# Kernel tuning notes

Hardware: AMD Instinct MI355X
Metric: run time of the kernel (lower is better)

Reference implementation:

```python
import jax, jax.numpy as jnp
import numpy as np

H = 512      # hidden_size
OUT = 1      # output_size (forced by prev_output shape (B,1,1))
B = 64       # batch
T = 1024     # output_length


def setup_inputs() -> dict:
    key = jax.random.key(0)
    ks = jax.random.split(key, 10)
    s_in = 1.0 / np.sqrt(H)
    return {
        "context_vector": jax.random.normal(ks[0], (B, 1, H), jnp.float32),
        "expected_output": jax.random.normal(ks[1], (B, T, OUT), jnp.float32),
        "W_ih0": jax.random.normal(ks[2], (3 * H, H + OUT), jnp.float32) * s_in,
        "W_hh0": jax.random.normal(ks[3], (3 * H, H), jnp.float32) * s_in,
        "b_ih0": jnp.zeros((3 * H,), jnp.float32),
        "b_hh0": jnp.zeros((3 * H,), jnp.float32),
        "W_ih1": jax.random.normal(ks[4], (3 * H, H), jnp.float32) * s_in,
        "W_hh1": jax.random.normal(ks[5], (3 * H, H), jnp.float32) * s_in,
        "b_ih1": jnp.zeros((3 * H,), jnp.float32),
        "b_hh1": jnp.zeros((3 * H,), jnp.float32),
        "W_o1": jax.random.normal(ks[6], (H, H), jnp.float32) * s_in,
        "b_o1": jnp.zeros((H,), jnp.float32),
        "W_o2": jax.random.normal(ks[7], (OUT, H), jnp.float32) * s_in,
        "b_o2": jnp.zeros((OUT,), jnp.float32),
        "force": 0,  # teacher forcing disabled (original uses python random -> nondeterministic)
    }


def _gru_cell(x, h, W_ih, W_hh, b_ih, b_hh):
    # PyTorch GRU cell math
    gi = x @ W_ih.T + b_ih          # (B, 3H)
    gh = h @ W_hh.T + b_hh          # (B, 3H)
    i_r, i_z, i_n = jnp.split(gi, 3, axis=-1)
    h_r, h_z, h_n = jnp.split(gh, 3, axis=-1)
    r = jax.nn.sigmoid(i_r + h_r)
    z = jax.nn.sigmoid(i_z + h_z)
    n = jnp.tanh(i_n + r * h_n)
    return (1.0 - z) * n + z * h


def reference(context_vector, expected_output, W_ih0, W_hh0, b_ih0, b_hh0,
              W_ih1, W_hh1, b_ih1, b_hh1, W_o1, b_o1, W_o2, b_o2, force):
    del force  # force=False path only (deterministic)
    batch = context_vector.shape[0]
    out_len = expected_output.shape[1]
    ctx = context_vector[:, 0, :]                      # (B, H)
    h0 = jnp.zeros((batch, H), context_vector.dtype)
    h1 = jnp.zeros((batch, H), context_vector.dtype)
    prev = jnp.zeros((batch, OUT), context_vector.dtype)

    def step(carry, _):
        h0, h1, prev = carry
        x = jnp.concatenate([ctx, prev], axis=1)       # (B, H+1)
        h0n = _gru_cell(x, h0, W_ih0, W_hh0, b_ih0, b_hh0)
        h1n = _gru_cell(h0n, h1, W_ih1, W_hh1, b_ih1, b_hh1)
        y = jax.nn.relu(h1n @ W_o1.T + b_o1)           # (B, H)
        y = jax.nn.relu(y @ W_o2.T + b_o2)             # (B, 1)
        return (h0n, h1n, y), y

    (h0, h1, _), ys = jax.lax.scan(step, (h0, h1, prev), None, length=out_len)
    outputs = jnp.transpose(ys, (1, 0, 2))             # (B, T, 1)
    h_i = jnp.stack([h0, h1], axis=0)                  # (n_layers, B, H)
    return outputs, h_i
```

## Files before the change

### kernel.cpp

```cpp
#include <hip/hip_runtime.h>
#include <stdint.h>


#define NWG 256
#define NT  256
#define TT  1024

typedef unsigned short ushort;
typedef unsigned int   uint;
typedef __attribute__((ext_vector_type(8))) short short8;
typedef __attribute__((ext_vector_type(4))) float f32x4;
typedef __attribute__((ext_vector_type(4))) uint  uint4v;

struct __align__(16) SmemR0 {
  ushort wpl[2][48*520];
  float  gictx[3*16*68];
  float  wcol[3][16];
  float  bhnN[16];
  float  prevS[64];
};
struct __align__(16) SmemR2 {
  ushort whh[2][48*520];
  ushort wih[48*520];
  float  xk[3][64][16];
  float  bsumR[16], bsumZ[16], binN[16], bhnN[16];
};
struct __align__(16) SmemR3 {
  ushort wpl[2][16*520];
  float  xk[2][64][4];
  float  bo1v[16], wo2v[16];
};

__device__ __forceinline__ float frcp(float x){
#if __has_builtin(__builtin_amdgcn_rcpf)
  return __builtin_amdgcn_rcpf(x);
#else
  return 1.f/x;
#endif
}
__device__ __forceinline__ float sigm(float x){ return frcp(1.f + __expf(-x)); }
__device__ __forceinline__ float tanh_f(float x){
  return 1.f - 2.f*frcp(__expf(2.f*x) + 1.f);
}
__device__ __forceinline__ float bf2f(ushort h){ return __uint_as_float(((uint)h)<<16); }
__device__ __forceinline__ ushort bfrnd(float x){
  uint u = __float_as_uint(x);
  return (ushort)((u + 0x7fffu + ((u>>16)&1u)) >> 16);
}
#define SWP(p, v)  (void)__hip_atomic_exchange((uint*)(p), (uint)(v), __ATOMIC_RELAXED, __HIP_MEMORY_SCOPE_AGENT)
#define ALD1(p)    __hip_atomic_load((const uint*)(p), __ATOMIC_RELAXED, __HIP_MEMORY_SCOPE_AGENT)
#define ALDF(p)    __uint_as_float(ALD1(p))
#define FADDI(p)   (void)__hip_atomic_fetch_add((p), 1, __ATOMIC_RELAXED, __HIP_MEMORY_SCOPE_AGENT)

__device__ __forceinline__ void gbar(int* slots, int* epoch, int w, int tid, int e){
  __syncthreads();
  if (tid == 0)
    __hip_atomic_store(&slots[w], e, __ATOMIC_RELEASE, __HIP_MEMORY_SCOPE_AGENT);
  if (w == 0 && tid < 64){
    for(;;){
      int m0 = __hip_atomic_load(&slots[tid*4+0], __ATOMIC_RELAXED, __HIP_MEMORY_SCOPE_AGENT);
      int m1 = __hip_atomic_load(&slots[tid*4+1], __ATOMIC_RELAXED, __HIP_MEMORY_SCOPE_AGENT);
      int m2 = __hip_atomic_load(&slots[tid*4+2], __ATOMIC_RELAXED, __HIP_MEMORY_SCOPE_AGENT);
      int m3 = __hip_atomic_load(&slots[tid*4+3], __ATOMIC_RELAXED, __HIP_MEMORY_SCOPE_AGENT);
      if (__all(min(min(m0,m1),min(m2,m3)) >= e)) break;
      __builtin_amdgcn_s_sleep(1);
    }
    if (tid == 0){
      __builtin_amdgcn_fence(__ATOMIC_ACQUIRE, "agent");
      __hip_atomic_store(epoch, e, __ATOMIC_RELEASE, __HIP_MEMORY_SCOPE_AGENT);
    }
  }
  if (tid == 0){
    while (__hip_atomic_load(epoch, __ATOMIC_RELAXED, __HIP_MEMORY_SCOPE_AGENT) < e)
      __builtin_amdgcn_s_sleep(1);
    __builtin_amdgcn_fence(__ATOMIC_ACQUIRE, "agent");
  }
  __syncthreads();
}

__device__ __forceinline__ void drain_sync(){
  __builtin_amdgcn_s_waitcnt(0);
  __syncthreads();
}
__device__ __forceinline__ void waitmail(const int* w, int target, int tid){
  if (tid == 0)
    while ((int)ALD1(w) < target) {}
  __syncthreads();
}
__device__ __forceinline__ void waitmail2(const int* a, const int* b, int target, int tid){
  if (tid == 0)
    while ((int)ALD1(a) < target || (int)ALD1(b) < target) {}
  __syncthreads();
}

#define LD1SCD(dst, addr) \
  asm volatile("global_load_dword %0, %1, off sc0 sc1" : "=v"(dst) : "v"(addr));
#define STSH(addr, val) \
  asm volatile("global_store_short %0, %1, off sc0 sc1" :: "v"(addr), "v"(val) : "memory");
#define ST4SC(addr, val) \
  asm volatile("global_store_dwordx4 %0, %1, off sc0 sc1" :: "v"(addr), "v"(val) : "memory");
#define LD4A(DST, P, OFS) \
  asm volatile("global_load_dwordx4 %0, %1, off sc0 sc1" : "=v"(DST) : "v"((P) + (OFS)));
#define VMBAR4(a,b,c,d) \
  asm volatile("s_waitcnt vmcnt(0)" : "+v"(a),"+v"(b),"+v"(c),"+v"(d));
#define VMBAR8(a,b,c,d,e,f,g,h) \
  asm volatile("s_waitcnt vmcnt(0)" \
               : "+v"(a),"+v"(b),"+v"(c),"+v"(d),"+v"(e),"+v"(f),"+v"(g),"+v"(h));

#define TAGM 0x00010001u
#define FOLDV(V) fo_ |= ((V.x^em_)&TAGM)|((V.y^em_)&TAGM)| \
                        ((V.z^em_)&TAGM)|((V.w^em_)&TAGM);
#define FOLD4(p)  FOLDV(p##0) FOLDV(p##1) FOLDV(p##2) FOLDV(p##3)
#define FOLD8(p)  FOLD4(p) FOLDV(p##4) FOLDV(p##5) FOLDV(p##6) FOLDV(p##7)
#define FOLD16(p) FOLD8(p) FOLDV(p##8) FOLDV(p##9) FOLDV(p##10) FOLDV(p##11) \
                  FOLDV(p##12) FOLDV(p##13) FOLDV(p##14) FOLDV(p##15)

#define MFMA_ __builtin_amdgcn_mfma_f32_16x16x32_bf16

#define DECL_HILO(PH, PL) \
  uint4v ha0,ha1,ha2,ha3,ha4,ha5,ha6,ha7,ha8,ha9,ha10,ha11,ha12,ha13,ha14,ha15; \
  uint4v la0,la1,la2,la3,la4,la5,la6,la7,la8,la9,la10,la11,la12,la13,la14,la15; \
  LD4A(ha0,PH,aoffB+0*32) LD4A(ha1,PH,aoffB+1*32) LD4A(ha2,PH,aoffB+2*32) LD4A(ha3,PH,aoffB+3*32) \
  LD4A(ha4,PH,aoffB+4*32) LD4A(ha5,PH,aoffB+5*32) LD4A(ha6,PH,aoffB+6*32) LD4A(ha7,PH,aoffB+7*32) \
  LD4A(ha8,PH,aoffB+8*32) LD4A(ha9,PH,aoffB+9*32) LD4A(ha10,PH,aoffB+10*32) LD4A(ha11,PH,aoffB+11*32) \
  LD4A(ha12,PH,aoffB+12*32) LD4A(ha13,PH,aoffB+13*32) LD4A(ha14,PH,aoffB+14*32) LD4A(ha15,PH,aoffB+15*32) \
  LD4A(la0,PL,aoffB+0*32) LD4A(la1,PL,aoffB+1*32) LD4A(la2,PL,aoffB+2*32) LD4A(la3,PL,aoffB+3*32) \
  LD4A(la4,PL,aoffB+4*32) LD4A(la5,PL,aoffB+5*32) LD4A(la6,PL,aoffB+6*32) LD4A(la7,PL,aoffB+7*32) \
  LD4A(la8,PL,aoffB+8*32) LD4A(la9,PL,aoffB+9*32) LD4A(la10,PL,aoffB+10*32) LD4A(la11,PL,aoffB+11*32) \
  LD4A(la12,PL,aoffB+12*32) LD4A(la13,PL,aoffB+13*32) LD4A(la14,PL,aoffB+14*32) LD4A(la15,PL,aoffB+15*32) \
  VMBAR8(ha0,ha1,ha2,ha3,ha4,ha5,ha6,ha7) \
  VMBAR8(ha8,ha9,ha10,ha11,ha12,ha13,ha14,ha15) \
  VMBAR8(la0,la1,la2,la3,la4,la5,la6,la7) \
  VMBAR8(la8,la9,la10,la11,la12,la13,la14,la15)

#define MS3F(i) { \
  short8 AH_ = __builtin_bit_cast(short8, ha##i); \
  short8 AL_ = __builtin_bit_cast(short8, la##i); \
  const int ko_ = (i)*32 + q*8; \
  short8 bh_ = *(const short8*)(&S0.wpl[0][(col)*520 + ko_]); \
  short8 bl_ = *(const short8*)(&S0.wpl[1][(col)*520 + ko_]); \
  acc0 = MFMA_(AH_, bh_, acc0, 0,0,0); \
  acc0 = MFMA_(AL_, bh_, acc0, 0,0,0); \
  acc0 = MFMA_(AH_, bl_, acc0, 0,0,0); \
  bh_ = *(const short8*)(&S0.wpl[0][(16+col)*520 + ko_]); \
  bl_ = *(const short8*)(&S0.wpl[1][(16+col)*520 + ko_]); \
  acc1 = MFMA_(AH_, bh_, acc1, 0,0,0); \
  acc1 = MFMA_(AL_, bh_, acc1, 0,0,0); \
  acc1 = MFMA_(AH_, bl_, acc1, 0,0,0); \
  bh_ = *(const short8*)(&S0.wpl[0][(32+col)*520 + ko_]); \
  bl_ = *(const short8*)(&S0.wpl[1][(32+col)*520 + ko_]); \
  acc2 = MFMA_(AH_, bh_, acc2, 0,0,0); \
  acc2 = MFMA_(AL_, bh_, acc2, 0,0,0); \
  acc2 = MFMA_(AH_, bl_, acc2, 0,0,0); }

#define GH1(i) { \
  short8 AH_ = __builtin_bit_cast(short8, ha##i); \
  short8 AL_ = __builtin_bit_cast(short8, la##i); \
  const int ko_ = kq + (i)*32 + q*8; \
  short8 bh_ = *(const short8*)(&S2.whh[0][(col)*520 + ko_]); \
  short8 bl_ = *(const short8*)(&S2.whh[1][(col)*520 + ko_]); \
  aR = MFMA_(AH_, bh_, aR, 0,0,0); \
  aR = MFMA_(AL_, bh_, aR, 0,0,0); \
  aR = MFMA_(AH_, bl_, aR, 0,0,0); \
  bh_ = *(const short8*)(&S2.whh[0][(16+col)*520 + ko_]); \
  bl_ = *(const short8*)(&S2.whh[1][(16+col)*520 + ko_]); \
  aZ = MFMA_(AH_, bh_, aZ, 0,0,0); \
  aZ = MFMA_(AL_, bh_, aZ, 0,0,0); \
  aZ = MFMA_(AH_, bl_, aZ, 0,0,0); \
  bh_ = *(const short8*)(&S2.whh[0][(32+col)*520 + ko_]); \
  bl_ = *(const short8*)(&S2.whh[1][(32+col)*520 + ko_]); \
  aNh = MFMA_(AH_, bh_, aNh, 0,0,0); \
  aNh = MFMA_(AL_, bh_, aNh, 0,0,0); \
  aNh = MFMA_(AH_, bl_, aNh, 0,0,0); }

#define GI1(i) { \
  short8 AH_ = __builtin_bit_cast(short8, ga##i); \
  const int ko_ = kq + (i)*32 + q*8; \
  short8 bh_ = *(const short8*)(&S2.wih[(col)*520 + ko_]); \
  aR = MFMA_(AH_, bh_, aR, 0,0,0); \
  bh_ = *(const short8*)(&S2.wih[(16+col)*520 + ko_]); \
  aZ = MFMA_(AH_, bh_, aZ, 0,0,0); \
  bh_ = *(const short8*)(&S2.wih[(32+col)*520 + ko_]); \
  aNi = MFMA_(AH_, bh_, aNi, 0,0,0); }

#define DECL_HI8(P) \
  uint4v ha0,ha1,ha2,ha3,ha4,ha5,ha6,ha7; \
  LD4A(ha0,P,aoff8+0*32) LD4A(ha1,P,aoff8+1*32) LD4A(ha2,P,aoff8+2*32) LD4A(ha3,P,aoff8+3*32) \
  LD4A(ha4,P,aoff8+4*32) LD4A(ha5,P,aoff8+5*32) LD4A(ha6,P,aoff8+6*32) LD4A(ha7,P,aoff8+7*32) \
  VMBAR8(ha0,ha1,ha2,ha3,ha4,ha5,ha6,ha7)

#define MS1H(i) { \
  short8 AH_ = __builtin_bit_cast(short8, ha##i); \
  const int ko_ = kb + (i)*32 + q*8; \
  short8 bh_ = *(const short8*)(&S3.wpl[0][(col)*520 + ko_]); \
  short8 bl_ = *(const short8*)(&S3.wpl[1][(col)*520 + ko_]); \
  acc0 = MFMA_(AH_, bh_, acc0, 0,0,0); \
  acc0 = MFMA_(AH_, bl_, acc0, 0,0,0); }

#define RUN16(M) M(0) M(1) M(2) M(3) M(4) M(5) M(6) M(7) \
                 M(8) M(9) M(10) M(11) M(12) M(13) M(14) M(15)
#define RUN8(M)  M(0) M(1) M(2) M(3) M(4) M(5) M(6) M(7)
#define RUN4(M)  M(0) M(1) M(2) M(3)

extern "C" __global__ void __launch_bounds__(NT, 1)
decoder_rnn(const float* __restrict__ ctx,
            const float* __restrict__ Wih0,
            const float* __restrict__ Whh0,
            const float* __restrict__ bih0,
            const float* __restrict__ bhh0g,
            const float* __restrict__ Wih1,
            const float* __restrict__ Whh1,
            const float* __restrict__ bih1g,
            const float* __restrict__ bhh1g,
            const float* __restrict__ Wo1,
            const float* __restrict__ bo1g,
            const float* __restrict__ Wo2,
            const float* __restrict__ bo2g,
            float* __restrict__ out,
            float* __restrict__ ws)
{
  extern __shared__ char smem_raw[];
  SmemR0& S0 = *reinterpret_cast<SmemR0*>(smem_raw);
  SmemR2& S2 = *reinterpret_cast<SmemR2*>(smem_raw);
  SmemR3& S3 = *reinterpret_cast<SmemR3*>(smem_raw);
  const int tid = threadIdx.x;
  const int wg  = blockIdx.x;

  ushort* hp  = (ushort*)ws;
  float* yout = (float*)ws + 196608;
  int*  ibase = (int*)((float*)ws + 200704);
  int* gslots = ibase;
  int* epoch  = ibase + 256;
  int* mbox   = ibase + 512;

  const float bo2v = bo2g[0];

  for (int i = wg*NT + tid; i < 200704; i += NWG*NT)
    SWP((uint*)ws + i, 0u);
  if (wg == 0)
    for (int i = tid; i < 256*32; i += NT) SWP(mbox + i, 0);

  const int gid   = wg >> 7;
  const int m     = wg & 127;
  const int bbase = 32*gid;
  int role, j, bh = 0;
  if (m < 32){ role = 0; j = m; }
  else if (m < 96){ role = 2; bh = (m - 32) >> 5; j = m & 31; }
  else { role = 3; j = m - 96; }

  if (role == 0){
    for (int i = tid; i < 48*512; i += NT){
      int r = i >> 9, k = i & 511;
      int g3 = r >> 4, n = r & 15;
      float wv = Whh0[(size_t)(g3*512 + 16*j + n)*512 + k];
      ushort hh = bfrnd(wv);
      S0.wpl[0][r*520 + k] = hh;
      S0.wpl[1][r*520 + k] = bfrnd(wv - bf2f(hh));
    }
    if (tid < 48){
      int g3 = tid >> 4, n = tid & 15;
      S0.wcol[g3][n] = Wih0[(size_t)(g3*512 + 16*j + n)*513 + 512];
    }
    if (tid < 16) S0.bhnN[tid] = bhh0g[2*512 + 16*j + tid];
    for (int idx = tid; idx < 1536; idx += NT){
      int r = idx >> 5, bl = idx & 31;
      int g3 = r >> 4, n = r & 15;
      int grow = g3*512 + 16*j + n;
      const float* wr = Wih0 + (size_t)grow*513;
      const float* cx = ctx  + (size_t)(bbase + bl)*512;
      float s = bih0[grow];
      if (g3 < 2) s += bhh0g[grow];
      #pragma unroll 4
      for (int k = 0; k < 512; ++k) s += wr[k]*cx[k];
      S0.gictx[g3*1088 + n*68 + bl] = s;
    }
  } else if (role == 2){
    for (int i = tid; i < 48*512; i += NT){
      int r = i >> 9, k = i & 511;
      int g3 = r >> 4, n = r & 15;
      size_t row = (size_t)(g3*512 + 16*j + n)*512 + k;
      float wv = Whh1[row];
      ushort hh = bfrnd(wv);
      S2.whh[0][r*520 + k] = hh;
      S2.whh[1][r*520 + k] = bfrnd(wv - bf2f(hh));
      S2.wih[r*520 + k] = bfrnd(Wih1[row]);
    }
    if (tid < 16){
      int n = tid;
      S2.bsumR[n] = bih1g[16*j + n]       + bhh1g[16*j + n];
      S2.bsumZ[n] = bih1g[512 + 16*j + n] + bhh1g[512 + 16*j + n];
      S2.binN[n]  = bih1g[1024 + 16*j + n];
      S2.bhnN[n]  = bhh1g[1024 + 16*j + n];
    }
  } else {
    for (int i = tid; i < 16*512; i += NT){
      int r = i >> 9, k = i & 511;
      float wv = Wo1[(size_t)(16*j + r)*512 + k];
      ushort hh = bfrnd(wv);
      S3.wpl[0][r*520 + k] = hh;
      S3.wpl[1][r*520 + k] = bfrnd(wv - bf2f(hh));
    }
    if (tid < 16){ S3.bo1v[tid] = bo1g[16*j + tid]; S3.wo2v[tid] = Wo2[16*j + tid]; }
  }

  gbar(gslots, epoch, wg, tid, 1);

  int* myline = mbox + wg*32;
  const int gb = gid*128;

  const int v   = tid >> 6;
  const int l   = tid & 63;
  const int q   = l >> 4;
  const int col = l & 15;
  const int ng  = 16*j + col;

  if (role == 0){
    const int bblk  = v & 1;
    const int aoffB = (bbase + 16*bblk + col)*512 + q*8;
    const int b0wL  = 16*bblk + 4*q;
    float hc0 = 0.f, hc1 = 0.f, hc2 = 0.f, hc3 = 0.f;
    for (int t = 0; t < TT; ++t){
      const int r0 = t & 1, w0 = r0 ^ 1;
      waitmail(myline + 0, 32*t, tid);
      const ushort* rH = hp + r0*32768;
      const ushort* rL = hp + 65536 + r0*32768;
      ushort*       wH = hp + w0*32768;
      ushort*       wL = hp + 65536 + w0*32768;
      f32x4 acc0={0,0,0,0}, acc1={0,0,0,0}, acc2={0,0,0,0};
      if (v < 2){
        const uint em_ = (t==0) ? 0u : (((((t-1)>>1)&1u)^1u) * TAGM);
        for(;;){
          DECL_HILO(rH, rL)
          uint fo_ = 0u;
          FOLD16(ha) FOLD16(la)
          if (__all((int)(fo_ == 0u))){ RUN16(MS3F) break; }
          __builtin_amdgcn_s_sleep(1);
        }
      }
      waitmail(myline + 1, 32*t, tid);
      if (v == 0){
        float s = 0.f;
        if (t > 0){
          const uint ey_ = (((t-1)>>1)&1u)^1u;
          const float* yp = yout + ((t-1)&1)*2048 + bbase + l;
          for(;;){
            float vv[32]; uint fo_ = 0u;
            if (l < 32){
              #pragma unroll
              for (int jj = 0; jj < 32; ++jj)
                LD1SCD(vv[jj], yp + jj*64)
              VMBAR8(vv[0],vv[1],vv[2],vv[3],vv[4],vv[5],vv[6],vv[7])
              VMBAR8(vv[8],vv[9],vv[10],vv[11],vv[12],vv[13],vv[14],vv[15])
              VMBAR8(vv[16],vv[17],vv[18],vv[19],vv[20],vv[21],vv[22],vv[23])
              VMBAR8(vv[24],vv[25],vv[26],vv[27],vv[28],vv[29],vv[30],vv[31])
              #pragma unroll
              for (int jj = 0; jj < 32; ++jj)
                fo_ |= (__float_as_uint(vv[jj]) ^ ey_) & 1u;
            }
            if (__all((int)(fo_ == 0u))){
              if (l < 32){
                #pragma unroll
                for (int st = 16; st >= 1; st >>= 1)
                  #pragma unroll
                  for (int k2 = 0; k2 < st; ++k2) vv[k2] += vv[k2 + st];
                s = vv[0];
              }
              break;
            }
            __builtin_amdgcn_s_sleep(1);
          }
        }
        if (l < 32){
          float pv = fmaxf(s + bo2v, 0.f);
          S0.prevS[l] = pv;
          if (j == 0 && t > 0) out[(size_t)(bbase + l)*TT + (t-1)] = pv;
        }
      }
      __syncthreads();
      if (v < 2){
        const uint tg0_ = ((t>>1)&1u)^1u;
        f32x4 pv4 = *(const f32x4*)&S0.prevS[b0wL];
        f32x4 gR = *(const f32x4*)&S0.gictx[0*1088 + col*68 + b0wL];
        f32x4 gZ = *(const f32x4*)&S0.gictx[1*1088 + col*68 + b0wL];
        f32x4 gN = *(const f32x4*)&S0.gictx[2*1088 + col*68 + b0wL];
        float wc0 = S0.wcol[0][col], wc1 = S0.wcol[1][col], wc2 = S0.wcol[2][col];
        float bhn = S0.bhnN[col];
        #define E0(i, HC) { \
          float rr = sigm(gR[i] + pv4[i]*wc0 + acc0[i]); \
          float zz = sigm(gZ[i] + pv4[i]*wc1 + acc1[i]); \
          float nn = tanh_f(gN[i] + pv4[i]*wc2 + rr*(acc2[i] + bhn)); \
          float h = (1.f-zz)*nn + zz*HC; \
          HC = h; \
          uint hu_ = ((uint)bfrnd(h) & 0xFFFEu) | tg0_; \
          uint lu_ = ((uint)bfrnd(h - bf2f((ushort)hu_)) & 0xFFFEu) | tg0_; \
          STSH(wH + (size_t)(bbase + b0wL + (i))*512 + ng, hu_) \
          STSH(wL + (size_t)(bbase + b0wL + (i))*512 + ng, lu_) }
        E0(0,hc0) E0(1,hc1) E0(2,hc2) E0(3,hc3)
        #undef E0
      }
      __syncthreads();
      if (tid < 96)
        FADDI(mbox + (gb + tid)*32 + 0);
    }
  } else if (role == 2){
    ushort* p1H = hp + 131072;
    ushort* p1L = hp + 163840;
    const int bb16  = bbase + 16*bh;
    const int kq    = v*128;
    const int aoffA = (bb16 + col)*512 + kq + q*8;
    float hc0 = 0.f, hc1 = 0.f, hc2 = 0.f, hc3 = 0.f;
    for (int t = 0; t < TT; ++t){
      waitmail(myline + 1 + bh, 32*t, tid);
      f32x4 aR={0,0,0,0}, aZ={0,0,0,0}, aNi={0,0,0,0}, aNh={0,0,0,0};
      {
        const uint em_ = (t==0) ? 0u : ((((t-1)&1u)^1u) * TAGM);
        for(;;){
          uint4v ha0,ha1,ha2,ha3, la0,la1,la2,la3;
          LD4A(ha0, p1H, aoffA+0*32) LD4A(ha1, p1H, aoffA+1*32)
          LD4A(ha2, p1H, aoffA+2*32) LD4A(ha3, p1H, aoffA+3*32)
          LD4A(la0, p1L, aoffA+0*32) LD4A(la1, p1L, aoffA+1*32)
          LD4A(la2, p1L, aoffA+2*32) LD4A(la3, p1L, aoffA+3*32)
          VMBAR8(ha0,ha1,ha2,ha3,la0,la1,la2,la3)
          uint fo_ = 0u;
          FOLD4(ha) FOLD4(la)
          if (__all((int)(fo_ == 0u))){ RUN4(GH1) break; }
          __builtin_amdgcn_s_sleep(1);
        }
      }
      waitmail(myline + 0, 32*(t+1), tid);
      {
        const uint em_ = (((t>>1)&1u)^1u) * TAGM;
        const ushort* rH = hp + ((t & 1) ^ 1)*32768;
        for(;;){
          uint4v ga0,ga1,ga2,ga3;
          LD4A(ga0, rH, aoffA+0*32) LD4A(ga1, rH, aoffA+1*32)
          LD4A(ga2, rH, aoffA+2*32) LD4A(ga3, rH, aoffA+3*32)
          VMBAR4(ga0,ga1,ga2,ga3)
          uint fo_ = 0u;
          FOLD4(ga)
          if (__all((int)(fo_ == 0u))){ RUN4(GI1) break; }
          __builtin_amdgcn_s_sleep(1);
        }
      }
      if (v >= 1){
        *(f32x4*)&S2.xk[v-1][l][0]  = aR;
        *(f32x4*)&S2.xk[v-1][l][4]  = aZ;
        *(f32x4*)&S2.xk[v-1][l][8]  = aNi;
        *(f32x4*)&S2.xk[v-1][l][12] = aNh;
      }
      __syncthreads();
      if (v == 0){
        const uint tg1_ = (t&1u)^1u;
        #pragma unroll
        for (int w = 0; w < 3; ++w){
          aR  += *(const f32x4*)&S2.xk[w][l][0];
          aZ  += *(const f32x4*)&S2.xk[w][l][4];
          aNi += *(const f32x4*)&S2.xk[w][l][8];
          aNh += *(const f32x4*)&S2.xk[w][l][12];
        }
        float bsR = S2.bsumR[col], bsZ = S2.bsumZ[col];
        float biN = S2.binN[col],  bhN = S2.bhnN[col];
        #define E1(i, HC) { \
          float r1 = sigm(aR[i] + bsR); \
          float z1 = sigm(aZ[i] + bsZ); \
          float n1 = tanh_f(aNi[i] + biN + r1*(aNh[i] + bhN)); \
          float h = (1.f-z1)*n1 + z1*HC; \
          HC = h; \
          uint hu_ = ((uint)bfrnd(h) & 0xFFFEu) | tg1_; \
          uint lu_ = ((uint)bfrnd(h - bf2f((ushort)hu_)) & 0xFFFEu) | tg1_; \
          STSH(p1H + (size_t)(bb16 + 4*q + (i))*512 + ng, hu_) \
          STSH(p1L + (size_t)(bb16 + 4*q + (i))*512 + ng, lu_) }
        E1(0,hc0) E1(1,hc1) E1(2,hc2) E1(3,hc3)
        #undef E1
      }
      __syncthreads();
      if (tid < 96)
        FADDI(mbox + (gb + 32 + tid)*32 + 1 + bh);
    }
  } else {
    const ushort* rH = hp + 131072;
    const int bblk  = v & 1;
    const int kb    = (v >> 1)*256;
    const int aoff8 = (bbase + 16*bblk + col)*512 + kb + q*8;
    const int b0wL  = 16*bblk + 4*q;
    for (int t = 0; t < TT; ++t){
      waitmail2(myline + 1, myline + 2, 32*(t+1), tid);
      f32x4 acc0={0,0,0,0};
      {
        const uint em_ = ((t&1u)^1u) * TAGM;
        for(;;){
          DECL_HI8(rH)
          uint fo_ = 0u;
          FOLD8(ha)
          if (__all((int)(fo_ == 0u))){ RUN8(MS1H) break; }
          __builtin_amdgcn_s_sleep(1);
        }
      }
      if (v >= 2)
        *(f32x4*)&S3.xk[bblk][l][0] = acc0;
      __syncthreads();
      if (v < 2){
        acc0 += *(const f32x4*)&S3.xk[bblk][l][0];
        float s0 = S3.wo2v[col]*fmaxf(acc0[0] + S3.bo1v[col], 0.f);
        float s1 = S3.wo2v[col]*fmaxf(acc0[1] + S3.bo1v[col], 0.f);
        float s2 = S3.wo2v[col]*fmaxf(acc0[2] + S3.bo1v[col], 0.f);
        float s3 = S3.wo2v[col]*fmaxf(acc0[3] + S3.bo1v[col], 0.f);
        #pragma unroll
        for (int d = 1; d < 16; d <<= 1){
          s0 += __shfl_xor(s0, d);
          s1 += __shfl_xor(s1, d);
          s2 += __shfl_xor(s2, d);
          s3 += __shfl_xor(s3, d);
        }
        if (col == 0){
          const uint tgy_ = ((t>>1)&1u)^1u;
          uint* rp = (uint*)(yout + (t&1)*2048 + j*64 + bbase + b0wL);
          uint4v uv = { (__float_as_uint(s0) & ~1u) | tgy_,
                        (__float_as_uint(s1) & ~1u) | tgy_,
                        (__float_as_uint(s2) & ~1u) | tgy_,
                        (__float_as_uint(s3) & ~1u) | tgy_ };
          ST4SC(rp, uv)
        }
      }
      __syncthreads();
      if (tid < 32)
        FADDI(mbox + (gb + tid)*32 + 1);
    }
  }

  drain_sync();
  gbar(gslots, epoch, wg, tid, 2);
  if (wg == 0 && tid < 64){
    float s = 0.f;
    const float* yp = yout + 2048 + tid;
    #pragma unroll
    for (int jj = 0; jj < 32; ++jj) s += ALDF(yp + jj*64);
    out[(size_t)tid*TT + 1023] = fmaxf(s + bo2v, 0.f);
  }
  {
    int g = wg*256 + tid;
    if (g < 32768) out[65536 + g] = bf2f(hp[g]) + bf2f(hp[65536 + g]);
    else {
      int g2 = g - 32768;
      out[65536 + g] = bf2f(hp[131072 + g2]) + bf2f(hp[163840 + g2]);
    }
  }
}

extern "C" void kernel_launch(void* const* d_in, const int* in_sizes, int n_in,
                              void* d_out, int out_size, void* d_ws, size_t ws_size,
                              hipStream_t stream){
  const float* ctx   = (const float*)d_in[0];
  const float* Wih0  = (const float*)d_in[2];
  const float* Whh0  = (const float*)d_in[3];
  const float* bih0  = (const float*)d_in[4];
  const float* bhh0  = (const float*)d_in[5];
  const float* Wih1  = (const float*)d_in[6];
  const float* Whh1  = (const float*)d_in[7];
  const float* bih1  = (const float*)d_in[8];
  const float* bhh1  = (const float*)d_in[9];
  const float* Wo1   = (const float*)d_in[10];
  const float* bo1   = (const float*)d_in[11];
  const float* Wo2   = (const float*)d_in[12];
  const float* bo2   = (const float*)d_in[13];

  (void)in_sizes; (void)n_in; (void)out_size; (void)ws_size;

  const int smem_sz = (int)sizeof(SmemR2);
  (void)hipFuncSetAttribute((const void*)decoder_rnn,
                            hipFuncAttributeMaxDynamicSharedMemorySize,
                            smem_sz);

  decoder_rnn<<<NWG, NT, smem_sz, stream>>>(
      ctx, Wih0, Whh0, bih0, bhh0, Wih1, Whh1, bih1, bhh1,
      Wo1, bo1, Wo2, bo2, (float*)d_out, (float*)d_ws);
}
```

Measured before the change: 8.451 ms.

## Replace mailbox counter handshakes with polling on tagged data canaries

Drops the per-step atomic mailbox counters, the fetch-add signals and the waitmail spins. In their place, thread 0 of each workgroup polls a single 16-byte canary from the parity-tagged hidden-state or output buffer that it will read next. This removes the atomic increments and an extra global round trip of signalling from the serial critical path of the recurrent loop. The canary check only sees one line of the producer's data, so readiness of the rest still depends on the existing full tag-fold retry loops.

```diff
diff --git a/kernel.cpp b/kernel.cpp
--- a/kernel.cpp
+++ b/kernel.cpp
@@ -50,7 +50,6 @@
 #define SWP(p, v)  (void)__hip_atomic_exchange((uint*)(p), (uint)(v), __ATOMIC_RELAXED, __HIP_MEMORY_SCOPE_AGENT)
 #define ALD1(p)    __hip_atomic_load((const uint*)(p), __ATOMIC_RELAXED, __HIP_MEMORY_SCOPE_AGENT)
 #define ALDF(p)    __uint_as_float(ALD1(p))
-#define FADDI(p)   (void)__hip_atomic_fetch_add((p), 1, __ATOMIC_RELAXED, __HIP_MEMORY_SCOPE_AGENT)
 
 __device__ __forceinline__ void gbar(int* slots, int* epoch, int w, int tid, int e){
   __syncthreads();
@@ -82,16 +81,6 @@
   __builtin_amdgcn_s_waitcnt(0);
   __syncthreads();
 }
-__device__ __forceinline__ void waitmail(const int* w, int target, int tid){
-  if (tid == 0)
-    while ((int)ALD1(w) < target) {}
-  __syncthreads();
-}
-__device__ __forceinline__ void waitmail2(const int* a, const int* b, int target, int tid){
-  if (tid == 0)
-    while ((int)ALD1(a) < target || (int)ALD1(b) < target) {}
-  __syncthreads();
-}
 
 #define LD1SCD(dst, addr) \
   asm volatile("global_load_dword %0, %1, off sc0 sc1" : "=v"(dst) : "v"(addr));
@@ -101,6 +90,8 @@
   asm volatile("global_store_dwordx4 %0, %1, off sc0 sc1" :: "v"(addr), "v"(val) : "memory");
 #define LD4A(DST, P, OFS) \
   asm volatile("global_load_dwordx4 %0, %1, off sc0 sc1" : "=v"(DST) : "v"((P) + (OFS)));
+#define VMBAR1(a)   asm volatile("s_waitcnt vmcnt(0)" : "+v"(a));
+#define VMBAR2(a,b) asm volatile("s_waitcnt vmcnt(0)" : "+v"(a),"+v"(b));
 #define VMBAR4(a,b,c,d) \
   asm volatile("s_waitcnt vmcnt(0)" : "+v"(a),"+v"(b),"+v"(c),"+v"(d));
 #define VMBAR8(a,b,c,d,e,f,g,h) \
@@ -114,6 +105,45 @@
 #define FOLD8(p)  FOLD4(p) FOLDV(p##4) FOLDV(p##5) FOLDV(p##6) FOLDV(p##7)
 #define FOLD16(p) FOLD8(p) FOLDV(p##8) FOLDV(p##9) FOLDV(p##10) FOLDV(p##11) \
                   FOLDV(p##12) FOLDV(p##13) FOLDV(p##14) FOLDV(p##15)
+
+__device__ __forceinline__ void waitcan(const ushort* p, uint em, int tid){
+  if (tid == 0){
+    for(;;){
+      uint4v c;
+      LD4A(c, (const uint*)p, 0)
+      VMBAR1(c)
+      uint fo = ((c.x^em)&TAGM)|((c.y^em)&TAGM)|((c.z^em)&TAGM)|((c.w^em)&TAGM);
+      if (fo == 0u) break;
+    }
+  }
+  __syncthreads();
+}
+__device__ __forceinline__ void waitcan2(const ushort* pa, const ushort* pb,
+                                         uint em, int tid){
+  if (tid == 0){
+    for(;;){
+      uint4v a, b;
+      LD4A(a, (const uint*)pa, 0)
+      LD4A(b, (const uint*)pb, 0)
+      VMBAR2(a, b)
+      uint fo = ((a.x^em)&TAGM)|((a.y^em)&TAGM)|((a.z^em)&TAGM)|((a.w^em)&TAGM)
+              | ((b.x^em)&TAGM)|((b.y^em)&TAGM)|((b.z^em)&TAGM)|((b.w^em)&TAGM);
+      if (fo == 0u) break;
+    }
+  }
+  __syncthreads();
+}
+__device__ __forceinline__ void waitcany(const float* p, uint ey, int tid){
+  if (tid == 0){
+    for(;;){
+      uint c;
+      asm volatile("global_load_dword %0, %1, off sc0 sc1" : "=v"(c) : "v"(p));
+      VMBAR1(c)
+      if (((c ^ ey) & 1u) == 0u) break;
+    }
+  }
+  __syncthreads();
+}
 
 #define MFMA_ __builtin_amdgcn_mfma_f32_16x16x32_bf16
 
@@ -231,14 +261,11 @@
   int*  ibase = (int*)((float*)ws + 200704);
   int* gslots = ibase;
   int* epoch  = ibase + 256;
-  int* mbox   = ibase + 512;
 
   const float bo2v = bo2g[0];
 
   for (int i = wg*NT + tid; i < 200704; i += NWG*NT)
     SWP((uint*)ws + i, 0u);
-  if (wg == 0)
-    for (int i = tid; i < 256*32; i += NT) SWP(mbox + i, 0);
 
   const int gid   = wg >> 7;
   const int m     = wg & 127;
@@ -305,9 +332,6 @@
 
   gbar(gslots, epoch, wg, tid, 1);
 
-  int* myline = mbox + wg*32;
-  const int gb = gid*128;
-
   const int v   = tid >> 6;
   const int l   = tid & 63;
   const int q   = l >> 4;
@@ -321,14 +345,15 @@
     float hc0 = 0.f, hc1 = 0.f, hc2 = 0.f, hc3 = 0.f;
     for (int t = 0; t < TT; ++t){
       const int r0 = t & 1, w0 = r0 ^ 1;
-      waitmail(myline + 0, 32*t, tid);
       const ushort* rH = hp + r0*32768;
       const ushort* rL = hp + 65536 + r0*32768;
       ushort*       wH = hp + w0*32768;
       ushort*       wL = hp + 65536 + w0*32768;
+      const uint emh = (t==0) ? 0u : (((((t-1)>>1)&1u)^1u) * TAGM);
+      waitcan(rH + (size_t)bbase*512, emh, tid);
       f32x4 acc0={0,0,0,0}, acc1={0,0,0,0}, acc2={0,0,0,0};
       if (v < 2){
-        const uint em_ = (t==0) ? 0u : (((((t-1)>>1)&1u)^1u) * TAGM);
+        const uint em_ = emh;
         for(;;){
           DECL_HILO(rH, rL)
           uint fo_ = 0u;
@@ -337,7 +362,8 @@
           __builtin_amdgcn_s_sleep(1);
         }
       }
-      waitmail(myline + 1, 32*t, tid);
+      if (t > 0)
+        waitcany(yout + ((t-1)&1)*2048 + bbase, (((t-1)>>1)&1u)^1u, tid);
       if (v == 0){
         float s = 0.f;
         if (t > 0){
@@ -398,9 +424,6 @@
         E0(0,hc0) E0(1,hc1) E0(2,hc2) E0(3,hc3)
         #undef E0
       }
-      __syncthreads();
-      if (tid < 96)
-        FADDI(mbox + (gb + tid)*32 + 0);
     }
   } else if (role == 2){
     ushort* p1H = hp + 131072;
@@ -410,10 +433,11 @@
     const int aoffA = (bb16 + col)*512 + kq + q*8;
     float hc0 = 0.f, hc1 = 0.f, hc2 = 0.f, hc3 = 0.f;
     for (int t = 0; t < TT; ++t){
-      waitmail(myline + 1 + bh, 32*t, tid);
+      const uint emA = (t==0) ? 0u : ((((t-1)&1u)^1u) * TAGM);
+      waitcan(p1H + (size_t)bb16*512, emA, tid);
       f32x4 aR={0,0,0,0}, aZ={0,0,0,0}, aNi={0,0,0,0}, aNh={0,0,0,0};
       {
-        const uint em_ = (t==0) ? 0u : ((((t-1)&1u)^1u) * TAGM);
+        const uint em_ = emA;
         for(;;){
           uint4v ha0,ha1,ha2,ha3, la0,la1,la2,la3;
           LD4A(ha0, p1H, aoffA+0*32) LD4A(ha1, p1H, aoffA+1*32)
@@ -427,10 +451,11 @@
           __builtin_amdgcn_s_sleep(1);
         }
       }
-      waitmail(myline + 0, 32*(t+1), tid);
+      const ushort* rH = hp + ((t & 1) ^ 1)*32768;
+      const uint emB = (((t>>1)&1u)^1u) * TAGM;
+      waitcan(rH + (size_t)bb16*512, emB, tid);
       {
-        const uint em_ = (((t>>1)&1u)^1u) * TAGM;
-        const ushort* rH = hp + ((t & 1) ^ 1)*32768;
+        const uint em_ = emB;
         for(;;){
           uint4v ga0,ga1,ga2,ga3;
           LD4A(ga0, rH, aoffA+0*32) LD4A(ga1, rH, aoffA+1*32)
@@ -474,8 +499,6 @@
         #undef E1
       }
       __syncthreads();
-      if (tid < 96)
-        FADDI(mbox + (gb + 32 + tid)*32 + 1 + bh);
     }
   } else {
     const ushort* rH = hp + 131072;
@@ -484,10 +507,11 @@
     const int aoff8 = (bbase + 16*bblk + col)*512 + kb + q*8;
     const int b0wL  = 16*bblk + 4*q;
     for (int t = 0; t < TT; ++t){
-      waitmail2(myline + 1, myline + 2, 32*(t+1), tid);
+      const uint emh1 = ((t&1u)^1u) * TAGM;
+      waitcan2(rH + (size_t)bbase*512, rH + (size_t)(bbase+16)*512, emh1, tid);
       f32x4 acc0={0,0,0,0};
       {
-        const uint em_ = ((t&1u)^1u) * TAGM;
+        const uint em_ = emh1;
         for(;;){
           DECL_HI8(rH)
           uint fo_ = 0u;
@@ -523,8 +547,6 @@
         }
       }
       __syncthreads();
-      if (tid < 32)
-        FADDI(mbox + (gb + tid)*32 + 1);
     }
   }
 
```

Result: no change. 8.297 ms (-1.8%).
